# Optimization experiments

Measured on AMD Instinct MI355X. Metric: run time of the kernel, lower is better.

The kernel has to match this reference:

```python
import jax, jax.numpy as jnp
import numpy as np

B, T, H, V = 256, 256, 512, 32000
L = 3  # stacked LSTM layers


def setup_inputs() -> dict:
    key = jax.random.key(0)
    ks = jax.random.split(key, 12)
    s = 0.05
    n = lambda k, shp: (jax.random.normal(k, shp, jnp.float32) * s)
    return {
        "text_1": jax.random.randint(ks[0], (B, T), 0, V, dtype=jnp.int32),
        "text_2": jax.random.randint(ks[1], (B, T), 0, V, dtype=jnp.int32),
        "text_3": jax.random.randint(ks[2], (B, T), 0, V, dtype=jnp.int32),
        "emb": n(ks[3], (V, H)),
        "Wx": n(ks[4], (L, H, 4 * H)),
        "Wh": n(ks[5], (L, H, 4 * H)),
        "b": jnp.zeros((L, 4 * H), jnp.float32),
        "g1": jnp.ones((3 * H,), jnp.float32), "beta1": jnp.zeros((3 * H,), jnp.float32),
        "W1": n(ks[6], (3 * H, 2 * H)), "bd1": jnp.zeros((2 * H,), jnp.float32),
        "g2": jnp.ones((2 * H,), jnp.float32), "beta2": jnp.zeros((2 * H,), jnp.float32),
        "W2": n(ks[7], (2 * H, H // 5)), "bd2": jnp.zeros((H // 5,), jnp.float32),
        "g3": jnp.ones((H // 5,), jnp.float32), "beta3": jnp.zeros((H // 5,), jnp.float32),
        "W3": n(ks[8], (H // 5, 4)), "bd3": jnp.zeros((4,), jnp.float32),
    }


def _lstm_stack(tokens, emb, Wx, Wh, b):
    # tokens: [B, T] int -> last hidden of top layer [B, H]
    x = emb[tokens]                      # [B, T, H]
    x = jnp.transpose(x, (1, 0, 2))      # [T, B, H] (scan over time)
    bsz, h = x.shape[1], Wh.shape[1]
    for l in range(Wx.shape[0]):
        Wx_l, Wh_l, b_l = Wx[l], Wh[l], b[l]
        def step(carry, xt):
            hprev, cprev = carry
            gates = xt @ Wx_l + hprev @ Wh_l + b_l      # [B, 4H]
            i, f, g, o = jnp.split(gates, 4, axis=-1)
            c = jax.nn.sigmoid(f) * cprev + jax.nn.sigmoid(i) * jnp.tanh(g)
            hnew = jax.nn.sigmoid(o) * jnp.tanh(c)
            return (hnew, c), hnew
        init = (jnp.zeros((bsz, h), x.dtype), jnp.zeros((bsz, h), x.dtype))
        _, x = jax.lax.scan(step, init, x)
    return x[-1]                          # rnn_output[:, -1, :]


def _bn(x, gamma, beta, eps=1e-3):
    m = jnp.mean(x, axis=0)
    v = jnp.var(x, axis=0)
    return gamma * (x - m) * jax.lax.rsqrt(v + eps) + beta


def reference(text_1, text_2, text_3, emb, Wx, Wh, b,
              g1, beta1, W1, bd1, g2, beta2, W2, bd2, g3, beta3, W3, bd3):
    r1 = _lstm_stack(text_1, emb, Wx, Wh, b)
    r2 = _lstm_stack(text_2, emb, Wx, Wh, b)
    r3 = _lstm_stack(text_3, emb, Wx, Wh, b)
    r = jnp.concatenate([r1, r2, r3], axis=1)   # [B, 3H]
    r = _bn(r, g1, beta1)
    r = jax.nn.selu(r @ W1 + bd1)
    r = _bn(r, g2, beta2)
    r = jax.nn.selu(r @ W2 + bd2)
    r = _bn(r, g3, beta3)
    return r @ W3 + bd3                          # [B, 4] logits
```

## Files before the change

### kernel.cpp

```cpp
#include <hip/hip_runtime.h>
#include <hip/hip_bf16.h>

typedef __attribute__((ext_vector_type(8))) short short8;
typedef __attribute__((ext_vector_type(4))) float floatx4;

namespace {
constexpr int kB1 = 256;
constexpr int kT  = 256;
constexpr int kH  = 512;
constexpr int kL  = 3;
constexpr int kB3 = 768;
constexpr int kK  = 1024;
constexpr int kN  = 2048;
constexpr size_t kHB = (size_t)kB3 * kH;

constexpr size_t WREP_OFF   = 0;
constexpr size_t WREP_BYTES = (size_t)kL * kK * kN * 2;
constexpr size_t BREP_OFF   = WREP_OFF + WREP_BYTES;
constexpr size_t BREP_BYTES = (size_t)kL * kN * 4;
constexpr size_t HBUF_OFF   = BREP_OFF + BREP_BYTES;
constexpr size_t HBUF_BYTES = (size_t)kL * 2 * kHB * 2;
constexpr size_t CBUF_OFF   = HBUF_OFF + HBUF_BYTES;
constexpr size_t CBUF_BYTES = (size_t)kL * kHB * 4;
constexpr size_t BNA_OFF    = CBUF_OFF + CBUF_BYTES;
constexpr size_t BNC_OFF    = BNA_OFF + 1536 * 4;
constexpr size_t Z1_OFF     = BNC_OFF + 1536 * 4;
constexpr size_t Z2_OFF     = Z1_OFF + (size_t)256 * 1024 * 4;
constexpr size_t FLAG_OFF   = Z2_OFF + (size_t)256 * 102 * 4;
constexpr size_t BAR_OFF    = FLAG_OFF + 128;
constexpr int kPersistGrid  = 768;
}

__device__ __forceinline__ float ldf(const void* p, size_t idx, int isf32) {
  if (isf32) return ((const float*)p)[idx];
  return __bfloat162float(((const __hip_bfloat16*)p)[idx]);
}

__device__ __forceinline__ short f2bs(float x) {
  union { __hip_bfloat16 h; short s; } u;
  u.h = __float2bfloat16(x);
  return u.s;
}

__device__ __forceinline__ short8 cvt8(const float* q) {
  float4 lo = *(const float4*)q;
  float4 hi = *(const float4*)(q + 4);
  short8 v;
  v[0] = f2bs(lo.x); v[1] = f2bs(lo.y); v[2] = f2bs(lo.z); v[3] = f2bs(lo.w);
  v[4] = f2bs(hi.x); v[5] = f2bs(hi.y); v[6] = f2bs(hi.z); v[7] = f2bs(hi.w);
  return v;
}

__global__ void detect_kernel(const unsigned* __restrict__ g1, int* __restrict__ flag,
                              unsigned* __restrict__ bar) {
  int tid = threadIdx.x;
  if (tid < 256)
    __hip_atomic_store(&bar[tid], 0u, __ATOMIC_RELAXED, __HIP_MEMORY_SCOPE_AGENT);
  if (tid == 0 && blockIdx.x == 0)
    *flag = (g1[0] == 0x3F800000u) ? 1 : 0;
}

__global__ __launch_bounds__(256) void repack_kernel(
    const void* __restrict__ Wx, const void* __restrict__ Wh,
    const void* __restrict__ bias, const int* __restrict__ flagp,
    __hip_bfloat16* __restrict__ Wrep, float* __restrict__ brep) {
  int isf32 = *flagp;
  int idx = blockIdx.x * 256 + threadIdx.x;
  if (idx >= kL * kK * kN) return;
  int j  = idx & 7;
  int n2 = (idx >> 3) & (kN - 1);
  int kg = (idx >> 14) & 127;
  int l  = idx >> 21;
  int k  = kg * 8 + j;
  int ntile = n2 >> 7, c = n2 & 127, g = c >> 5, ul = c & 31;
  int u = ntile * 32 + ul;
  int col = g * 512 + u;
  float v;
  if (k < kH) v = ldf(Wx, ((size_t)l * kH + k) * kN + col, isf32);
  else        v = ldf(Wh, ((size_t)l * kH + (k - kH)) * kN + col, isf32);
  Wrep[idx] = __float2bfloat16(v);
  if (kg == 0 && j == 0) brep[l * kN + n2] = ldf(bias, (size_t)l * kN + col, isf32);
}

__device__ __forceinline__ void grid_barrier(unsigned* bar, int bid, int tid) {
  __syncthreads();
  if (tid == 0) {
    unsigned* cnt  = bar + (bid & 7) * 16;
    unsigned* gcnt = bar + 128;
    unsigned* gen  = bar + 160;
    unsigned g = __hip_atomic_load(gen, __ATOMIC_RELAXED, __HIP_MEMORY_SCOPE_AGENT);
    unsigned a = __hip_atomic_fetch_add(cnt, 1u, __ATOMIC_ACQ_REL, __HIP_MEMORY_SCOPE_AGENT);
    if (a == (kPersistGrid / 8) - 1u) {
      __hip_atomic_store(cnt, 0u, __ATOMIC_RELAXED, __HIP_MEMORY_SCOPE_AGENT);
      unsigned ga = __hip_atomic_fetch_add(gcnt, 1u, __ATOMIC_ACQ_REL, __HIP_MEMORY_SCOPE_AGENT);
      if (ga == 7u) {
        __hip_atomic_store(gcnt, 0u, __ATOMIC_RELAXED, __HIP_MEMORY_SCOPE_AGENT);
        __hip_atomic_store(gen, g + 1u, __ATOMIC_RELEASE, __HIP_MEMORY_SCOPE_AGENT);
      }
    }
    long long t0 = (long long)__builtin_amdgcn_s_memrealtime();
    while (__hip_atomic_load(gen, __ATOMIC_RELAXED, __HIP_MEMORY_SCOPE_AGENT) == g) {
      __builtin_amdgcn_s_sleep(2);
      if ((long long)__builtin_amdgcn_s_memrealtime() - t0 > 20000000LL) break;
    }
  }
  __syncthreads();
  __builtin_amdgcn_fence(__ATOMIC_ACQUIRE, "agent");
}

__global__ __launch_bounds__(256, 3) void persist_kernel(
    const __hip_bfloat16* __restrict__ Wrep, const float* __restrict__ brep,
    __hip_bfloat16* __restrict__ hbuf, const void* __restrict__ emb,
    const int* __restrict__ flagp, const int* __restrict__ t1,
    const int* __restrict__ t2, const int* __restrict__ t3,
    unsigned* __restrict__ bar) {
  __shared__ __align__(16) char smem[26624];

  const int tid = threadIdx.x;
  const int bid = blockIdx.x;
  const int l   = bid >> 8;
  const int mt  = (bid >> 4) & 15;
  const int nt  = bid & 15;
  const int wv = tid >> 6, lane = tid & 63, lm = lane & 15, lq = lane >> 4;
  const int isf32 = *flagp;
  const int r0   = tid >> 4;
  const int c16  = tid & 15;
  const int kcol = c16 * 8;

  const int R0 = mt * 48 + r0, R1 = R0 + 16, R2 = R0 + 32;
  const int* tb0 = nullptr; const int* tb1 = nullptr; const int* tb2 = nullptr;
  int tk0 = 0, tk1 = 0, tk2 = 0;
  if (l == 0) {
    tb0 = (((R0 >> 8) == 0) ? t1 : ((R0 >> 8) == 1) ? t2 : t3) + (R0 & 255) * kT;
    tb1 = (((R1 >> 8) == 0) ? t1 : ((R1 >> 8) == 1) ? t2 : t3) + (R1 & 255) * kT;
    tb2 = (((R2 >> 8) == 0) ? t1 : ((R2 >> 8) == 1) ? t2 : t3) + (R2 & 255) * kT;
    tk0 = tb0[0]; tk1 = tb1[0]; tk2 = tb2[0];
  }
  const unsigned ro0 = (unsigned)R0 * kH + kcol;
  const unsigned ro1 = (unsigned)R1 * kH + kcol;
  const unsigned ro2 = (unsigned)R2 * kH + kcol;

  const __hip_bfloat16* WB = Wrep + (size_t)l * kK * kN;
  const int n0w = nt * 128 + wv * 32;
  const float bv0 = brep[l * kN + n0w + lm];
  const float bv1 = brep[l * kN + n0w + 16 + lm];

  char* aw0 = smem + r0 * 256 + ((c16 ^ (r0 & 7)) << 4);
  char* aw1 = aw0 + 16 * 256;
  char* aw2 = aw0 + 32 * 256;
  const char* arb = smem + lm * 256;
  int oswz[4];
#pragma unroll
  for (int kk = 0; kk < 4; kk++) oswz[kk] = (((kk * 4 + lq) ^ (lm & 7)) << 4);

  const int cuu = tid & 31, crow = tid >> 5;
  float creg[6] = {0.f, 0.f, 0.f, 0.f, 0.f, 0.f};

  short8 aA0, aA1, aA2, aB0, aB1, aB2;
  short8 bA[4][2], bB[4][2];

#pragma unroll 1
  for (int s = 0; s < kT + kL - 1; s++) {
    const int t = s - l;
    if (t >= 0 && t < kT) {
      const __hip_bfloat16* hp = hbuf + ((size_t)l * 2 + ((t & 1) ^ 1)) * kHB;
      const __hip_bfloat16* xh = nullptr;
      const void *xe0 = nullptr, *xe1 = nullptr, *xe2 = nullptr;
      int nk0 = 0, nk1 = 0, nk2 = 0;
      if (l == 0) {
        if (isf32) {
          xe0 = (const void*)((const float*)emb + (size_t)tk0 * kH + kcol);
          xe1 = (const void*)((const float*)emb + (size_t)tk1 * kH + kcol);
          xe2 = (const void*)((const float*)emb + (size_t)tk2 * kH + kcol);
        } else {
          xe0 = (const void*)((const __hip_bfloat16*)emb + (size_t)tk0 * kH + kcol);
          xe1 = (const void*)((const __hip_bfloat16*)emb + (size_t)tk1 * kH + kcol);
          xe2 = (const void*)((const __hip_bfloat16*)emb + (size_t)tk2 * kH + kcol);
        }
        if (t + 1 < kT) { nk0 = tb0[t + 1]; nk1 = tb1[t + 1]; nk2 = tb2[t + 1]; }
      } else {
        xh = hbuf + ((size_t)(l - 1) * 2 + (t & 1)) * kHB;
      }

      auto loadA = [&](int sl, short8& d0, short8& d1, short8& d2) {
        if (sl < 4) {
          if (l == 0) {
            if (isf32) {
              d0 = cvt8((const float*)xe0 + sl * 128);
              d1 = cvt8((const float*)xe1 + sl * 128);
              d2 = cvt8((const float*)xe2 + sl * 128);
            } else {
              d0 = *(const short8*)((const __hip_bfloat16*)xe0 + sl * 128);
              d1 = *(const short8*)((const __hip_bfloat16*)xe1 + sl * 128);
              d2 = *(const short8*)((const __hip_bfloat16*)xe2 + sl * 128);
            }
          } else {
            d0 = *(const short8*)(xh + ro0 + sl * 128);
            d1 = *(const short8*)(xh + ro1 + sl * 128);
            d2 = *(const short8*)(xh + ro2 + sl * 128);
          }
        } else if (t == 0) {
          short8 z = {0, 0, 0, 0, 0, 0, 0, 0};
          d0 = z; d1 = z; d2 = z;
        } else {
          d0 = *(const short8*)(hp + ro0 + (sl - 4) * 128);
          d1 = *(const short8*)(hp + ro1 + (sl - 4) * 128);
          d2 = *(const short8*)(hp + ro2 + (sl - 4) * 128);
        }
      };
      auto loadB = [&](int sl, short8 (&bf)[4][2]) {
#pragma unroll
        for (int kk = 0; kk < 4; kk++)
#pragma unroll
          for (int nf = 0; nf < 2; nf++) {
            int kg = sl * 16 + kk * 4 + lq;
            bf[kk][nf] = *(const short8*)(WB + ((size_t)kg * kN + n0w + nf * 16 + lm) * 8);
          }
      };

      if (l != 0 || t == 0) loadA(0, aA0, aA1, aA2);
      if (t == 0) loadB(0, bA);

      floatx4 zf = {0.f, 0.f, 0.f, 0.f};
      floatx4 acc[3][2];
#pragma unroll
      for (int a = 0; a < 3; a++) { acc[a][0] = zf; acc[a][1] = zf; }

#pragma unroll
      for (int sl = 0; sl < 8; sl++) {
        __syncthreads();
        if ((sl & 1) == 0) { *(short8*)aw0 = aA0; *(short8*)aw1 = aA1; *(short8*)aw2 = aA2; }
        else               { *(short8*)aw0 = aB0; *(short8*)aw1 = aB1; *(short8*)aw2 = aB2; }
        __syncthreads();
        if (sl < 7) {
          if ((sl & 1) == 0) { loadA(sl + 1, aB0, aB1, aB2); loadB(sl + 1, bB); }
          else               { loadA(sl + 1, aA0, aA1, aA2); loadB(sl + 1, bA); }
        }
#pragma unroll
        for (int kk = 0; kk < 4; kk++) {
          const short8* bf = (sl & 1) ? &bB[kk][0] : &bA[kk][0];
          short8 af0 = *(const short8*)(arb + 0 * 4096 + oswz[kk]);
          short8 af1 = *(const short8*)(arb + 1 * 4096 + oswz[kk]);
          short8 af2 = *(const short8*)(arb + 2 * 4096 + oswz[kk]);
          acc[0][0] = __builtin_amdgcn_mfma_f32_16x16x32_bf16(af0, bf[0], acc[0][0], 0, 0, 0);
          acc[0][1] = __builtin_amdgcn_mfma_f32_16x16x32_bf16(af0, bf[1], acc[0][1], 0, 0, 0);
          acc[1][0] = __builtin_amdgcn_mfma_f32_16x16x32_bf16(af1, bf[0], acc[1][0], 0, 0, 0);
          acc[1][1] = __builtin_amdgcn_mfma_f32_16x16x32_bf16(af1, bf[1], acc[1][1], 0, 0, 0);
          acc[2][0] = __builtin_amdgcn_mfma_f32_16x16x32_bf16(af2, bf[0], acc[2][0], 0, 0, 0);
          acc[2][1] = __builtin_amdgcn_mfma_f32_16x16x32_bf16(af2, bf[1], acc[2][1], 0, 0, 0);
        }
      }

      __syncthreads();
      float* gl = (float*)smem;
#pragma unroll
      for (int mf = 0; mf < 3; mf++)
#pragma unroll
        for (int nf = 0; nf < 2; nf++)
#pragma unroll
          for (int r = 0; r < 4; r++) {
            int rowf = mf * 16 + lq * 4 + r;
            gl[(wv * 48 + rowf) * 34 + nf * 16 + lm] = acc[mf][nf][r] + (nf ? bv1 : bv0);
          }
      __syncthreads();

      __hip_bfloat16* hout = hbuf + ((size_t)l * 2 + (t & 1)) * kHB;
#pragma unroll
      for (int ii = 0; ii < 6; ii++) {
        int rowf = crow + 8 * ii;
        float gi = fminf(fmaxf(gl[(0 * 48 + rowf) * 34 + cuu], -40.f), 40.f);
        float gf = fminf(fmaxf(gl[(1 * 48 + rowf) * 34 + cuu], -40.f), 40.f);
        float gg = fminf(fmaxf(gl[(2 * 48 + rowf) * 34 + cuu], -40.f), 40.f);
        float go = fminf(fmaxf(gl[(3 * 48 + rowf) * 34 + cuu], -40.f), 40.f);
        float c_old = (t > 0) ? creg[ii] : 0.f;
        float si = 1.f / (1.f + __expf(-gi));
        float sf = 1.f / (1.f + __expf(-gf));
        float so = 1.f / (1.f + __expf(-go));
        float cn = sf * c_old + si * tanhf(gg);
        float hn = so * tanhf(cn);
        creg[ii] = cn;
        union { __hip_bfloat16 h; unsigned short u; } cv;
        cv.h = __float2bfloat16(hn);
        __hip_atomic_store(
            (unsigned short*)(hout + (size_t)(mt * 48 + rowf) * kH + nt * 32 + cuu),
            cv.u, __ATOMIC_RELAXED, __HIP_MEMORY_SCOPE_AGENT);
      }

      if (t + 1 < kT) {
        loadB(0, bA);
        if (l == 0) {
          tk0 = nk0; tk1 = nk1; tk2 = nk2;
          if (isf32) {
            xe0 = (const void*)((const float*)emb + (size_t)tk0 * kH + kcol);
            xe1 = (const void*)((const float*)emb + (size_t)tk1 * kH + kcol);
            xe2 = (const void*)((const float*)emb + (size_t)tk2 * kH + kcol);
          } else {
            xe0 = (const void*)((const __hip_bfloat16*)emb + (size_t)tk0 * kH + kcol);
            xe1 = (const void*)((const __hip_bfloat16*)emb + (size_t)tk1 * kH + kcol);
            xe2 = (const void*)((const __hip_bfloat16*)emb + (size_t)tk2 * kH + kcol);
          }
          loadA(0, aA0, aA1, aA2);
        }
      }
    }
    if (s < kT + kL - 2) grid_barrier(bar, bid, tid);
  }
}

__global__ __launch_bounds__(256) void step_kernel(
    int s,
    const __hip_bfloat16* __restrict__ Wrep, const float* __restrict__ brep,
    __hip_bfloat16* __restrict__ hbuf, float* __restrict__ cbuf,
    const void* __restrict__ emb, const int* __restrict__ flagp,
    const int* __restrict__ t1, const int* __restrict__ t2, const int* __restrict__ t3) {
  __shared__ __align__(16) char smem[34816];

  int bid = blockIdx.x;
  int l  = bid / 192;
  int rr = bid % 192;
  int nt = rr & 15;
  int mt = rr >> 4;
  int t = s - l;
  if (t < 0 || t >= kT) return;

  int isf32 = *flagp;
  int tid = threadIdx.x;
  int wv = tid >> 6, lane = tid & 63;
  int lm = lane & 15, lq = lane >> 4;

  int arow = tid >> 2;
  int kc   = tid & 3;
  int row_g = mt * 64 + arow;

  const void* xsrc;
  bool xf32 = false;
  if (l == 0) {
    int i = row_g >> 8, bb = row_g & 255;
    const int* txt = (i == 0) ? t1 : (i == 1) ? t2 : t3;
    int tok = txt[bb * kT + t];
    if (isf32) { xsrc = (const void*)((const float*)emb + (size_t)tok * kH); xf32 = true; }
    else         xsrc = (const void*)((const __hip_bfloat16*)emb + (size_t)tok * kH);
  } else {
    const __hip_bfloat16* hIn = hbuf + ((size_t)(l - 1) * 2 + (t & 1)) * kHB;
    xsrc = (const void*)(hIn + (size_t)row_g * kH);
  }
  const __hip_bfloat16* hrow = nullptr;
  if (t > 0) {
    const __hip_bfloat16* hPrev = hbuf + ((size_t)l * 2 + ((t & 1) ^ 1)) * kHB;
    hrow = hPrev + (size_t)row_g * kH;
  }

  floatx4 zf = {0.f, 0.f, 0.f, 0.f};
  floatx4 acc[4][2];
#pragma unroll
  for (int a = 0; a < 4; a++)
#pragma unroll
    for (int b = 0; b < 2; b++) acc[a][b] = zf;

  const __hip_bfloat16* WB = Wrep + (size_t)l * kK * kN;
  int n0w = nt * 128 + wv * 32;

#pragma unroll 1
  for (int sl = 0; sl < 8; sl++) {
    short8 bfrag[4][2];
#pragma unroll
    for (int kk = 0; kk < 4; kk++)
#pragma unroll
      for (int nf = 0; nf < 2; nf++) {
        size_t kg = (size_t)(sl * 16 + kk * 4 + lq);
        const __hip_bfloat16* p = WB + (kg * kN + (n0w + nf * 16 + lm)) * 8;
        bfrag[kk][nf] = *(const short8*)p;
      }
    short8 av[4];
    bool zero = (sl >= 4) && (t == 0);
    if (!zero) {
      if (sl < 4 && xf32) {
        const float* sf = (const float*)xsrc + sl * 128;
#pragma unroll
        for (int jj = 0; jj < 4; jj++) {
          const float* q = sf + kc * 8 + jj * 32;
          float4 lo = *(const float4*)q;
          float4 hi = *(const float4*)(q + 4);
          short8 v;
          v[0] = f2bs(lo.x); v[1] = f2bs(lo.y); v[2] = f2bs(lo.z); v[3] = f2bs(lo.w);
          v[4] = f2bs(hi.x); v[5] = f2bs(hi.y); v[6] = f2bs(hi.z); v[7] = f2bs(hi.w);
          av[jj] = v;
        }
      } else {
        const __hip_bfloat16* src = (sl < 4)
            ? ((const __hip_bfloat16*)xsrc + sl * 128)
            : (hrow + (sl - 4) * 128);
#pragma unroll
        for (int jj = 0; jj < 4; jj++)
          av[jj] = *(const short8*)(src + kc * 8 + jj * 32);
      }
    } else {
      short8 vz = {0, 0, 0, 0, 0, 0, 0, 0};
#pragma unroll
      for (int jj = 0; jj < 4; jj++) av[jj] = vz;
    }
    __syncthreads();
#pragma unroll
    for (int jj = 0; jj < 4; jj++) {
      int klocal = kc * 8 + jj * 32;
      *(short8*)(smem + arow * 272 + klocal * 2) = av[jj];
    }
    __syncthreads();
#pragma unroll
    for (int kk = 0; kk < 4; kk++) {
      short8 afrag[4];
#pragma unroll
      for (int mf = 0; mf < 4; mf++) {
        int rowf = mf * 16 + lm;
        afrag[mf] = *(const short8*)(smem + rowf * 272 + kk * 64 + lq * 16);
      }
#pragma unroll
      for (int mf = 0; mf < 4; mf++)
#pragma unroll
        for (int nf = 0; nf < 2; nf++)
          acc[mf][nf] = __builtin_amdgcn_mfma_f32_16x16x32_bf16(
              afrag[mf], bfrag[kk][nf], acc[mf][nf], 0, 0, 0);
    }
  }

  const float* bl = brep + l * kN;
#pragma unroll
  for (int nf = 0; nf < 2; nf++) {
    float bv = bl[n0w + nf * 16 + lm];
#pragma unroll
    for (int mf = 0; mf < 4; mf++)
#pragma unroll
      for (int r = 0; r < 4; r++) acc[mf][nf][r] += bv;
  }

  __syncthreads();
  float* gl = (float*)smem;
#pragma unroll
  for (int mf = 0; mf < 4; mf++)
#pragma unroll
    for (int nf = 0; nf < 2; nf++)
#pragma unroll
      for (int r = 0; r < 4; r++) {
        int rowf = mf * 16 + lq * 4 + r;
        int uu   = nf * 16 + lm;
        gl[((size_t)wv * 64 + rowf) * 34 + uu] = acc[mf][nf][r];
      }
  __syncthreads();

  float* cl = cbuf + (size_t)l * kHB;
  __hip_bfloat16* hout = hbuf + ((size_t)l * 2 + (t & 1)) * kHB;
#pragma unroll
  for (int ii = 0; ii < 8; ii++) {
    int idx = tid + 256 * ii;
    int uu = idx & 31, rowf = idx >> 5;
    float gi = fminf(fmaxf(gl[(0 * 64 + rowf) * 34 + uu], -40.f), 40.f);
    float gf = fminf(fmaxf(gl[(1 * 64 + rowf) * 34 + uu], -40.f), 40.f);
    float gg = fminf(fmaxf(gl[(2 * 64 + rowf) * 34 + uu], -40.f), 40.f);
    float go = fminf(fmaxf(gl[(3 * 64 + rowf) * 34 + uu], -40.f), 40.f);
    int bg = mt * 64 + rowf;
    int ug = nt * 32 + uu;
    size_t off = (size_t)bg * kH + ug;
    float c_old = (t > 0) ? cl[off] : 0.f;
    float si = 1.f / (1.f + __expf(-gi));
    float sf = 1.f / (1.f + __expf(-gf));
    float so = 1.f / (1.f + __expf(-go));
    float cn = sf * c_old + si * tanhf(gg);
    float hn = so * tanhf(cn);
    cl[off] = cn;
    hout[off] = __float2bfloat16(hn);
  }
}

__global__ __launch_bounds__(256) void stats_kernel(
    int ncols, int mode, const void* __restrict__ src,
    const void* __restrict__ gamma, const void* __restrict__ beta,
    const int* __restrict__ flagp, float* __restrict__ bn_a, float* __restrict__ bn_c) {
  int isf32 = *flagp;
  int col = blockIdx.x * 256 + threadIdx.x;
  if (col >= ncols) return;
  float sum = 0.f, ss = 0.f;
  for (int b = 0; b < kB1; b++) {
    float v;
    if (mode == 0) {
      const __hip_bfloat16* h = (const __hip_bfloat16*)src;
      v = __bfloat162float(h[((size_t)((col >> 9) * kB1 + b)) * kH + (col & 511)]);
    } else {
      v = ((const float*)src)[(size_t)b * ncols + col];
    }
    v = fmaxf(-1e15f, fminf(v, 1e15f));
    sum += v; ss += v * v;
  }
  float mean = sum * (1.f / kB1);
  float var  = ss * (1.f / kB1) - mean * mean;
  float a = ldf(gamma, col, isf32) * rsqrtf(var + 1e-3f);
  bn_a[col] = a;
  bn_c[col] = ldf(beta, col, isf32) - mean * a;
}

__global__ __launch_bounds__(256) void headgemm_kernel(
    int Kd, int Nd, int mode, const void* __restrict__ Asrc,
    const float* __restrict__ bn_a, const float* __restrict__ bn_c,
    const void* __restrict__ W, const void* __restrict__ bias,
    const int* __restrict__ flagp, float* __restrict__ out, int do_selu) {
  __shared__ float As[32][65];
  __shared__ float Bs[32][65];
  int isf32 = *flagp;
  int tid = threadIdx.x;
  int bx = blockIdx.x, by = blockIdx.y;
  int tx = tid & 15, ty = tid >> 4;
  float acc[4][4] = {};
  int am = tid & 63, ak = tid >> 6;
  int bk = tid >> 3, bn8 = (tid & 7) * 8;
  for (int ks = 0; ks < Kd; ks += 32) {
    __syncthreads();
    for (int jj = 0; jj < 8; jj++) {
      int kl = ak * 8 + jj;
      int kg = ks + kl;
      int mg = by * 64 + am;
      float v;
      if (mode == 0) {
        const __hip_bfloat16* h = (const __hip_bfloat16*)Asrc;
        v = __bfloat162float(h[((size_t)((kg >> 9) * kB1 + mg)) * kH + (kg & 511)]);
      } else {
        v = ((const float*)Asrc)[(size_t)mg * Kd + kg];
      }
      As[kl][am] = v * bn_a[kg] + bn_c[kg];
    }
    for (int e = 0; e < 8; e++) {
      int col = bx * 64 + bn8 + e;
      Bs[bk][bn8 + e] = (col < Nd) ? ldf(W, (size_t)(ks + bk) * Nd + col, isf32) : 0.f;
    }
    __syncthreads();
    for (int k = 0; k < 32; k++) {
      float ar[4], br[4];
#pragma unroll
      for (int i = 0; i < 4; i++) ar[i] = As[k][ty * 4 + i];
#pragma unroll
      for (int j = 0; j < 4; j++) br[j] = Bs[k][tx * 4 + j];
#pragma unroll
      for (int i = 0; i < 4; i++)
#pragma unroll
        for (int j = 0; j < 4; j++) acc[i][j] += ar[i] * br[j];
    }
  }
  for (int i = 0; i < 4; i++) {
    int row = by * 64 + ty * 4 + i;
    for (int j = 0; j < 4; j++) {
      int col = bx * 64 + tx * 4 + j;
      if (col < Nd) {
        float y = acc[i][j] + ldf(bias, col, isf32);
        if (do_selu)
          y = (y > 0.f) ? 1.0507009873554805f * y
                        : 1.0507009873554805f * 1.6732632423543772f * (__expf(y) - 1.f);
        out[(size_t)row * Nd + col] = y;
      }
    }
  }
}

__global__ __launch_bounds__(256) void final_kernel(
    const float* __restrict__ z2, const float* __restrict__ bn_a, const float* __restrict__ bn_c,
    const void* __restrict__ W3, const void* __restrict__ bd3,
    const int* __restrict__ flagp, void* __restrict__ out) {
  int isf32 = *flagp;
  int b = threadIdx.x;
  float acc[4] = {0.f, 0.f, 0.f, 0.f};
  for (int j = 0; j < 102; j++) {
    float y = z2[b * 102 + j] * bn_a[j] + bn_c[j];
#pragma unroll
    for (int g = 0; g < 4; g++) acc[g] += y * ldf(W3, j * 4 + g, isf32);
  }
#pragma unroll
  for (int g = 0; g < 4; g++) {
    float y = acc[g] + ldf(bd3, g, isf32);
    if (isf32) ((float*)out)[b * 4 + g] = y;
    else ((__hip_bfloat16*)out)[b * 4 + g] = __float2bfloat16(y);
  }
}

extern "C" void kernel_launch(void* const* d_in, const int* in_sizes, int n_in,
                              void* d_out, int out_size, void* d_ws, size_t ws_size,
                              hipStream_t stream) {
  const int* t1 = (const int*)d_in[0];
  const int* t2 = (const int*)d_in[1];
  const int* t3 = (const int*)d_in[2];
  const void* emb = d_in[3];
  const void* Wx  = d_in[4];
  const void* Wh  = d_in[5];
  const void* bb  = d_in[6];
  const void* g1  = d_in[7];
  const void* be1 = d_in[8];
  const void* W1  = d_in[9];
  const void* bd1 = d_in[10];
  const void* g2  = d_in[11];
  const void* be2 = d_in[12];
  const void* W2  = d_in[13];
  const void* bd2 = d_in[14];
  const void* g3  = d_in[15];
  const void* be3 = d_in[16];
  const void* W3  = d_in[17];
  const void* bd3 = d_in[18];

  char* ws = (char*)d_ws;
  __hip_bfloat16* Wrep = (__hip_bfloat16*)(ws + WREP_OFF);
  float* brep = (float*)(ws + BREP_OFF);
  __hip_bfloat16* hbuf = (__hip_bfloat16*)(ws + HBUF_OFF);
  float* cbuf = (float*)(ws + CBUF_OFF);
  float* bn_a = (float*)(ws + BNA_OFF);
  float* bn_c = (float*)(ws + BNC_OFF);
  float* z1 = (float*)(ws + Z1_OFF);
  float* z2 = (float*)(ws + Z2_OFF);
  int* flag = (int*)(ws + FLAG_OFF);
  unsigned* bar = (unsigned*)(ws + BAR_OFF);

  static int persist_ok = -1;
  if (persist_ok < 0) {
    int nb = 0, ncu = 0, dev = 0;
    (void)hipGetDevice(&dev);
    (void)hipDeviceGetAttribute(&ncu, hipDeviceAttributeMultiprocessorCount, dev);
    hipError_t e = hipOccupancyMaxActiveBlocksPerMultiprocessor(&nb, persist_kernel, 256, 0);
    persist_ok = (e == hipSuccess && (long)nb * (long)ncu >= kPersistGrid) ? 1 : 0;
  }

  detect_kernel<<<1, 256, 0, stream>>>((const unsigned*)g1, flag, bar);

  repack_kernel<<<(kL * kK * kN) / 256, 256, 0, stream>>>(Wx, Wh, bb, flag, Wrep, brep);

  if (persist_ok) {
    persist_kernel<<<kPersistGrid, 256, 0, stream>>>(
        Wrep, brep, hbuf, emb, flag, t1, t2, t3, bar);
  } else {
    for (int s = 0; s < kT + kL - 1; s++)
      step_kernel<<<3 * 192, 256, 0, stream>>>(s, Wrep, brep, hbuf, cbuf, emb, flag, t1, t2, t3);
  }

  const __hip_bfloat16* hTop = hbuf + (2 * 2 + 1) * kHB;
  stats_kernel<<<6, 256, 0, stream>>>(1536, 0, hTop, g1, be1, flag, bn_a, bn_c);
  headgemm_kernel<<<dim3(16, 4), 256, 0, stream>>>(1536, 1024, 0, hTop, bn_a, bn_c, W1, bd1, flag, z1, 1);
  stats_kernel<<<4, 256, 0, stream>>>(1024, 1, z1, g2, be2, flag, bn_a, bn_c);
  headgemm_kernel<<<dim3(2, 4), 256, 0, stream>>>(1024, 102, 1, z1, bn_a, bn_c, W2, bd2, flag, z2, 1);
  stats_kernel<<<1, 256, 0, stream>>>(102, 1, z2, g3, be3, flag, bn_a, bn_c);
  final_kernel<<<1, 256, 0, stream>>>(z2, bn_a, bn_c, W3, bd3, flag, (void*)d_out);
}
```

Measured before the change: 6.011 ms.

## Use h ring buffer to skip most barrier acquire fences, remap blocks per XCD

The two-slot hidden-state double buffer becomes a 16-slot ring per layer. The agent-scope acquire fence after each grid barrier now runs only every 12th step, relying on the ring so that stale cached lines are never reread before an invalidation. Blocks are remapped so each XCD holds a chosen mix of layers and tiles. The embedding table is also pre-converted to bf16 by a new kernel, which removes the per-step dtype branches. Skipping the fences on most steps risks reading stale hidden state across XCD caches, and the ring and the bf16 table need extra workspace.

```diff
diff --git a/kernel.cpp b/kernel.cpp
--- a/kernel.cpp
+++ b/kernel.cpp
@@ -12,14 +12,19 @@
 constexpr int kB3 = 768;
 constexpr int kK  = 1024;
 constexpr int kN  = 2048;
+constexpr int kV  = 32000;
 constexpr size_t kHB = (size_t)kB3 * kH;
+constexpr int kRing = 16;
+constexpr int kFenceP = 12;
 
 constexpr size_t WREP_OFF   = 0;
 constexpr size_t WREP_BYTES = (size_t)kL * kK * kN * 2;
 constexpr size_t BREP_OFF   = WREP_OFF + WREP_BYTES;
 constexpr size_t BREP_BYTES = (size_t)kL * kN * 4;
-constexpr size_t HBUF_OFF   = BREP_OFF + BREP_BYTES;
-constexpr size_t HBUF_BYTES = (size_t)kL * 2 * kHB * 2;
+constexpr size_t EMB_OFF    = BREP_OFF + BREP_BYTES;
+constexpr size_t EMB_BYTES  = (size_t)kV * kH * 2;
+constexpr size_t HBUF_OFF   = EMB_OFF + EMB_BYTES;
+constexpr size_t HBUF_BYTES = (size_t)kL * kRing * kHB * 2;
 constexpr size_t CBUF_OFF   = HBUF_OFF + HBUF_BYTES;
 constexpr size_t CBUF_BYTES = (size_t)kL * kHB * 4;
 constexpr size_t BNA_OFF    = CBUF_OFF + CBUF_BYTES;
@@ -28,6 +33,7 @@
 constexpr size_t Z2_OFF     = Z1_OFF + (size_t)256 * 1024 * 4;
 constexpr size_t FLAG_OFF   = Z2_OFF + (size_t)256 * 102 * 4;
 constexpr size_t BAR_OFF    = FLAG_OFF + 128;
+constexpr size_t WS_NEEDED  = BAR_OFF + 1024;
 constexpr int kPersistGrid  = 768;
 }
 
@@ -82,7 +88,17 @@
   if (kg == 0 && j == 0) brep[l * kN + n2] = ldf(bias, (size_t)l * kN + col, isf32);
 }
 
-__device__ __forceinline__ void grid_barrier(unsigned* bar, int bid, int tid) {
+__global__ __launch_bounds__(256) void embrep_kernel(
+    const void* __restrict__ emb, const int* __restrict__ flagp,
+    __hip_bfloat16* __restrict__ er) {
+  int isf32 = *flagp;
+  size_t base = ((size_t)blockIdx.x * 256 + threadIdx.x) * 8;
+  if (base >= (size_t)kV * kH) return;
+  if (isf32) *(short8*)(er + base) = cvt8((const float*)emb + base);
+  else       *(short8*)(er + base) = *(const short8*)((const __hip_bfloat16*)emb + base);
+}
+
+__device__ __forceinline__ void grid_barrier(unsigned* bar, int bid, int tid, bool fence) {
   __syncthreads();
   if (tid == 0) {
     unsigned* cnt  = bar + (bid & 7) * 16;
@@ -105,12 +121,13 @@
     }
   }
   __syncthreads();
-  __builtin_amdgcn_fence(__ATOMIC_ACQUIRE, "agent");
+  if (fence)
+    __builtin_amdgcn_fence(__ATOMIC_ACQUIRE, "agent");
 }
 
 __global__ __launch_bounds__(256, 3) void persist_kernel(
     const __hip_bfloat16* __restrict__ Wrep, const float* __restrict__ brep,
-    __hip_bfloat16* __restrict__ hbuf, const void* __restrict__ emb,
+    __hip_bfloat16* __restrict__ hbuf, const __hip_bfloat16* __restrict__ er,
     const int* __restrict__ flagp, const int* __restrict__ t1,
     const int* __restrict__ t2, const int* __restrict__ t3,
     unsigned* __restrict__ bar) {
@@ -118,11 +135,15 @@
 
   const int tid = threadIdx.x;
   const int bid = blockIdx.x;
-  const int l   = bid >> 8;
-  const int mt  = (bid >> 4) & 15;
-  const int nt  = bid & 15;
+  const int xcd = bid & 7;
+  const int jj_ = bid >> 3;
+  const int l   = jj_ >> 5;
+  const int rr_ = jj_ & 31;
+  const int cmb = (xcd - 3 * l) & 7;
+  const int mt  = (cmb >> 2) * 8 + (rr_ >> 2);
+  const int nt  = (cmb & 3) * 4 + (rr_ & 3);
+
   const int wv = tid >> 6, lane = tid & 63, lm = lane & 15, lq = lane >> 4;
-  const int isf32 = *flagp;
   const int r0   = tid >> 4;
   const int c16  = tid & 15;
   const int kcol = c16 * 8;
@@ -158,42 +179,32 @@
 
   short8 aA0, aA1, aA2, aB0, aB1, aB2;
   short8 bA[4][2], bB[4][2];
+  const __hip_bfloat16 *xe0 = nullptr, *xe1 = nullptr, *xe2 = nullptr;
+  if (l == 0) {
+    xe0 = er + (size_t)tk0 * kH + kcol;
+    xe1 = er + (size_t)tk1 * kH + kcol;
+    xe2 = er + (size_t)tk2 * kH + kcol;
+  }
 
 #pragma unroll 1
   for (int s = 0; s < kT + kL - 1; s++) {
     const int t = s - l;
     if (t >= 0 && t < kT) {
-      const __hip_bfloat16* hp = hbuf + ((size_t)l * 2 + ((t & 1) ^ 1)) * kHB;
+      const __hip_bfloat16* hp = hbuf + ((size_t)l * kRing + ((t + kRing - 1) & (kRing - 1))) * kHB;
       const __hip_bfloat16* xh = nullptr;
-      const void *xe0 = nullptr, *xe1 = nullptr, *xe2 = nullptr;
       int nk0 = 0, nk1 = 0, nk2 = 0;
       if (l == 0) {
-        if (isf32) {
-          xe0 = (const void*)((const float*)emb + (size_t)tk0 * kH + kcol);
-          xe1 = (const void*)((const float*)emb + (size_t)tk1 * kH + kcol);
-          xe2 = (const void*)((const float*)emb + (size_t)tk2 * kH + kcol);
-        } else {
-          xe0 = (const void*)((const __hip_bfloat16*)emb + (size_t)tk0 * kH + kcol);
-          xe1 = (const void*)((const __hip_bfloat16*)emb + (size_t)tk1 * kH + kcol);
-          xe2 = (const void*)((const __hip_bfloat16*)emb + (size_t)tk2 * kH + kcol);
-        }
         if (t + 1 < kT) { nk0 = tb0[t + 1]; nk1 = tb1[t + 1]; nk2 = tb2[t + 1]; }
       } else {
-        xh = hbuf + ((size_t)(l - 1) * 2 + (t & 1)) * kHB;
+        xh = hbuf + ((size_t)(l - 1) * kRing + (t & (kRing - 1))) * kHB;
       }
 
       auto loadA = [&](int sl, short8& d0, short8& d1, short8& d2) {
         if (sl < 4) {
           if (l == 0) {
-            if (isf32) {
-              d0 = cvt8((const float*)xe0 + sl * 128);
-              d1 = cvt8((const float*)xe1 + sl * 128);
-              d2 = cvt8((const float*)xe2 + sl * 128);
-            } else {
-              d0 = *(const short8*)((const __hip_bfloat16*)xe0 + sl * 128);
-              d1 = *(const short8*)((const __hip_bfloat16*)xe1 + sl * 128);
-              d2 = *(const short8*)((const __hip_bfloat16*)xe2 + sl * 128);
-            }
+            d0 = *(const short8*)(xe0 + sl * 128);
+            d1 = *(const short8*)(xe1 + sl * 128);
+            d2 = *(const short8*)(xe2 + sl * 128);
           } else {
             d0 = *(const short8*)(xh + ro0 + sl * 128);
             d1 = *(const short8*)(xh + ro1 + sl * 128);
@@ -264,7 +275,7 @@
           }
       __syncthreads();
 
-      __hip_bfloat16* hout = hbuf + ((size_t)l * 2 + (t & 1)) * kHB;
+      __hip_bfloat16* hout = hbuf + ((size_t)l * kRing + (t & (kRing - 1))) * kHB;
 #pragma unroll
       for (int ii = 0; ii < 6; ii++) {
         int rowf = crow + 8 * ii;
@@ -290,20 +301,15 @@
         loadB(0, bA);
         if (l == 0) {
           tk0 = nk0; tk1 = nk1; tk2 = nk2;
-          if (isf32) {
-            xe0 = (const void*)((const float*)emb + (size_t)tk0 * kH + kcol);
-            xe1 = (const void*)((const float*)emb + (size_t)tk1 * kH + kcol);
-            xe2 = (const void*)((const float*)emb + (size_t)tk2 * kH + kcol);
-          } else {
-            xe0 = (const void*)((const __hip_bfloat16*)emb + (size_t)tk0 * kH + kcol);
-            xe1 = (const void*)((const __hip_bfloat16*)emb + (size_t)tk1 * kH + kcol);
-            xe2 = (const void*)((const __hip_bfloat16*)emb + (size_t)tk2 * kH + kcol);
-          }
+          xe0 = er + (size_t)tk0 * kH + kcol;
+          xe1 = er + (size_t)tk1 * kH + kcol;
+          xe2 = er + (size_t)tk2 * kH + kcol;
           loadA(0, aA0, aA1, aA2);
         }
       }
     }
-    if (s < kT + kL - 2) grid_barrier(bar, bid, tid);
+    if (s < kT + kL - 2)
+      grid_barrier(bar, bid, tid, (s % kFenceP) == (kFenceP - 1));
   }
 }
 
@@ -341,12 +347,12 @@
     if (isf32) { xsrc = (const void*)((const float*)emb + (size_t)tok * kH); xf32 = true; }
     else         xsrc = (const void*)((const __hip_bfloat16*)emb + (size_t)tok * kH);
   } else {
-    const __hip_bfloat16* hIn = hbuf + ((size_t)(l - 1) * 2 + (t & 1)) * kHB;
+    const __hip_bfloat16* hIn = hbuf + ((size_t)(l - 1) * kRing + (t & (kRing - 1))) * kHB;
     xsrc = (const void*)(hIn + (size_t)row_g * kH);
   }
   const __hip_bfloat16* hrow = nullptr;
   if (t > 0) {
-    const __hip_bfloat16* hPrev = hbuf + ((size_t)l * 2 + ((t & 1) ^ 1)) * kHB;
+    const __hip_bfloat16* hPrev = hbuf + ((size_t)l * kRing + ((t + kRing - 1) & (kRing - 1))) * kHB;
     hrow = hPrev + (size_t)row_g * kH;
   }
 
@@ -448,7 +454,7 @@
   __syncthreads();
 
   float* cl = cbuf + (size_t)l * kHB;
-  __hip_bfloat16* hout = hbuf + ((size_t)l * 2 + (t & 1)) * kHB;
+  __hip_bfloat16* hout = hbuf + ((size_t)l * kRing + (t & (kRing - 1))) * kHB;
 #pragma unroll
   for (int ii = 0; ii < 8; ii++) {
     int idx = tid + 256 * ii;
@@ -592,10 +598,10 @@
   const void* be1 = d_in[8];
   const void* W1  = d_in[9];
   const void* bd1 = d_in[10];
+  const void* W2  = d_in[13];
+  const void* bd2 = d_in[14];
   const void* g2  = d_in[11];
   const void* be2 = d_in[12];
-  const void* W2  = d_in[13];
-  const void* bd2 = d_in[14];
   const void* g3  = d_in[15];
   const void* be3 = d_in[16];
   const void* W3  = d_in[17];
@@ -604,6 +610,7 @@
   char* ws = (char*)d_ws;
   __hip_bfloat16* Wrep = (__hip_bfloat16*)(ws + WREP_OFF);
   float* brep = (float*)(ws + BREP_OFF);
+  __hip_bfloat16* embrep = (__hip_bfloat16*)(ws + EMB_OFF);
   __hip_bfloat16* hbuf = (__hip_bfloat16*)(ws + HBUF_OFF);
   float* cbuf = (float*)(ws + CBUF_OFF);
   float* bn_a = (float*)(ws + BNA_OFF);
@@ -619,22 +626,24 @@
     (void)hipGetDevice(&dev);
     (void)hipDeviceGetAttribute(&ncu, hipDeviceAttributeMultiprocessorCount, dev);
     hipError_t e = hipOccupancyMaxActiveBlocksPerMultiprocessor(&nb, persist_kernel, 256, 0);
-    persist_ok = (e == hipSuccess && (long)nb * (long)ncu >= kPersistGrid) ? 1 : 0;
+    persist_ok = (e == hipSuccess && (long)nb * (long)ncu >= kPersistGrid &&
+                  ws_size >= WS_NEEDED) ? 1 : 0;
   }
 
   detect_kernel<<<1, 256, 0, stream>>>((const unsigned*)g1, flag, bar);
 
   repack_kernel<<<(kL * kK * kN) / 256, 256, 0, stream>>>(Wx, Wh, bb, flag, Wrep, brep);
+  embrep_kernel<<<(kV * kH) / (256 * 8), 256, 0, stream>>>(emb, flag, embrep);
 
   if (persist_ok) {
     persist_kernel<<<kPersistGrid, 256, 0, stream>>>(
-        Wrep, brep, hbuf, emb, flag, t1, t2, t3, bar);
+        Wrep, brep, hbuf, embrep, flag, t1, t2, t3, bar);
   } else {
     for (int s = 0; s < kT + kL - 1; s++)
       step_kernel<<<3 * 192, 256, 0, stream>>>(s, Wrep, brep, hbuf, cbuf, emb, flag, t1, t2, t3);
   }
 
-  const __hip_bfloat16* hTop = hbuf + (2 * 2 + 1) * kHB;
+  const __hip_bfloat16* hTop = hbuf + (size_t)(2 * kRing + ((kT - 1) & (kRing - 1))) * kHB;
   stats_kernel<<<6, 256, 0, stream>>>(1536, 0, hTop, g1, be1, flag, bn_a, bn_c);
   headgemm_kernel<<<dim3(16, 4), 256, 0, stream>>>(1536, 1024, 0, hTop, bn_a, bn_c, W1, bd1, flag, z1, 1);
   stats_kernel<<<4, 256, 0, stream>>>(1024, 1, z1, g2, be2, flag, bn_a, bn_c);
```

Result: no change. 6.060 ms (+0.8%).
